# Performance work log

Hardware: AMD Instinct MI355X
Metric: run time of the kernel (lower is better)

## Reference

```python
import jax, jax.numpy as jnp
import numpy as np

N = 100_000      # nodes
E = 1_600_000    # edges (avg degree 16)
D_IN = 128
D_H = 128
D_P = 128
D_OUT = 64


def setup_inputs() -> dict:
    key = jax.random.key(0)
    ks = jax.random.split(key, 10)
    x = jax.random.normal(ks[0], (N, D_IN), dtype=jnp.float32)
    edge_index = jax.random.randint(ks[1], (2, E), 0, N, dtype=jnp.int64)
    # Mix_Pass layer 0: Linear(in->hidden, bias=False) + separate bias (zero-init)
    W1 = jax.random.normal(ks[2], (D_H, D_IN), dtype=jnp.float32) * 0.05
    b1 = jnp.zeros((D_H,), dtype=jnp.float32)
    # Mix_Pass layer 1: hidden->hidden
    W2 = jax.random.normal(ks[3], (D_H, D_H), dtype=jnp.float32) * 0.05
    b2 = jnp.zeros((D_H,), dtype=jnp.float32)
    # projection MLP
    fcW1 = jax.random.normal(ks[4], (D_P, D_H), dtype=jnp.float32) * 0.05
    fcb1 = jnp.zeros((D_P,), dtype=jnp.float32)
    fcW2 = jax.random.normal(ks[5], (D_OUT, D_P), dtype=jnp.float32) * 0.05
    fcb2 = jnp.zeros((D_OUT,), dtype=jnp.float32)
    return dict(x=x, edge_index=edge_index, W1=W1, b1=b1, W2=W2, b2=b2,
                fcW1=fcW1, fcb1=fcb1, fcW2=fcW2, fcb2=fcb2)


def _gcn_norm_with_self_loops(edge_index, n_nodes):
    # add_self_loops then gcn_norm (sym, improved=False, loops already added)
    loop = jnp.arange(n_nodes, dtype=edge_index.dtype)
    row = jnp.concatenate([edge_index[0], loop])  # source
    col = jnp.concatenate([edge_index[1], loop])  # target
    ew = jnp.ones(row.shape[0], dtype=jnp.float32)
    deg = jax.ops.segment_sum(ew, col, num_segments=n_nodes)
    dinv = jnp.where(deg > 0, jax.lax.rsqrt(deg), 0.0)
    return row, col, dinv[row] * ew * dinv[col]


def _mix_pass(z, W, b, row, col, ew, n_nodes):
    z = z @ W.T                                   # [N, out]
    msg = ew[:, None] * z[row]                    # gather source feats, scale
    out = jax.ops.segment_sum(msg, col, num_segments=n_nodes)  # scatter-add
    return out + b


def reference(x, edge_index, W1, b1, W2, b2, fcW1, fcb1, fcW2, fcb2):
    n_nodes = x.shape[0]
    row, col, ew = _gcn_norm_with_self_loops(edge_index, n_nodes)
    # dropout is identity in eval mode
    z = jax.nn.relu(_mix_pass(x, W1, b1, row, col, ew, n_nodes))
    zs = _mix_pass(z, W2, b2, row, col, ew, n_nodes)
    # project: elu(fc1) -> log_softmax(fc2)
    h = jax.nn.elu(zs @ fcW1.T + fcb1)
    res = jax.nn.log_softmax(h @ fcW2.T + fcb2, axis=1)
    return zs, res
```

## Files before the change

### kernel.cpp

```cpp
#include <hip/hip_runtime.h>
#include <hip/hip_bf16.h>

typedef __bf16 bf16_t;
typedef bf16_t bf16x8 __attribute__((ext_vector_type(8)));
typedef bf16_t bf16x4 __attribute__((ext_vector_type(4)));
typedef bf16_t bf16x2 __attribute__((ext_vector_type(2)));
typedef float f32x4 __attribute__((ext_vector_type(4)));

#define DEG_CAP 64

__device__ __forceinline__ void cvt4(const float* __restrict__ s, bf16_t* __restrict__ d, int i) {
    f32x4 v = ((const f32x4*)s)[i];
    bf16x4 o;
#pragma unroll
    for (int j = 0; j < 4; ++j) o[j] = (bf16_t)v[j];
    ((bf16x4*)d)[i] = o;
}

__global__ void setup_k(const float* xf, bf16_t* Xbf, int nx4,
                        const float* W1f, bf16_t* W1b,
                        const float* W2f, bf16_t* W2b,
                        const float* fW1f, bf16_t* fW1b,
                        const float* fW2f, bf16_t* fW2b,
                        int* cnt, int N) {
    int i = blockIdx.x * blockDim.x + threadIdx.x;
    if (i < nx4) { cvt4(xf, Xbf, i); return; }
    i -= nx4;
    if (i < 4096) { cvt4(W1f, W1b, i); return; }
    i -= 4096;
    if (i < 4096) { cvt4(W2f, W2b, i); return; }
    i -= 4096;
    if (i < 4096) { cvt4(fW1f, fW1b, i); return; }
    i -= 4096;
    if (i < 2048) { cvt4(fW2f, fW2b, i); return; }
    i -= 2048;
    if (i < N) cnt[i] = 0;
}

__device__ __forceinline__ void edge_rc(const int* __restrict__ ei, int E, int e,
                                        int N, int& r, int& c) {
    bool i64 = (ei[1] == 0) & (ei[3] == 0) & (ei[5] == 0) & (ei[7] == 0);
    int rr, cc;
    if (i64) { rr = ei[2 * e]; cc = ei[2 * E + 2 * e]; }
    else     { rr = ei[e];     cc = ei[E + e]; }
    r = ((unsigned)rr < (unsigned)N) ? rr : 0;
    c = ((unsigned)cc < (unsigned)N) ? cc : 0;
}

__global__ void countplace_k(const int* __restrict__ ei, int* __restrict__ cnt,
                             int* __restrict__ srcx, int E, int N) {
    int e = blockIdx.x * blockDim.x + threadIdx.x;
    if (e >= E) return;
    int r, c;
    edge_rc(ei, E, e, N, r, c);
    int p = atomicAdd(&cnt[c], 1);
    if (p < DEG_CAP) srcx[(size_t)c * DEG_CAP + p] = r;
}

template <int RELU, int WF32>
__global__ __launch_bounds__(256) void gather_k(const bf16_t* __restrict__ Y,
                                                const int* __restrict__ cnt,
                                                const int* __restrict__ srcx,
                                                const float* __restrict__ bias,
                                                bf16_t* __restrict__ out,
                                                float* __restrict__ out2, int n) {
    int node = blockIdx.x * 4 + (threadIdx.x >> 6);
    if (node >= n) return;
    int lane = threadIdx.x & 63;
    int f = lane * 2;
    int c = cnt[node];
    float di = rsqrtf((float)c + 1.0f);
    int cg = (c < DEG_CAP) ? c : DEG_CAP;
    const int* sl = srcx + (size_t)node * DEG_CAP;
    bf16x2 ys = *(const bf16x2*)(Y + (size_t)node * 128 + f);
    float a0 = (float)ys[0];
    float a1 = (float)ys[1];

    int e = 0;
    int end16 = cg & ~15;
    for (; e < end16; e += 16) {
        int s[16];
#pragma unroll
        for (int j = 0; j < 16; ++j) s[j] = sl[e + j];
        bf16x2 y[16];
#pragma unroll
        for (int j = 0; j < 16; ++j) y[j] = *(const bf16x2*)(Y + (size_t)s[j] * 128 + f);
#pragma unroll
        for (int j = 0; j < 16; ++j) { a0 += (float)y[j][0]; a1 += (float)y[j][1]; }
    }
    int end4 = cg & ~3;
    for (; e < end4; e += 4) {
        int s[4];
#pragma unroll
        for (int j = 0; j < 4; ++j) s[j] = sl[e + j];
        bf16x2 y[4];
#pragma unroll
        for (int j = 0; j < 4; ++j) y[j] = *(const bf16x2*)(Y + (size_t)s[j] * 128 + f);
#pragma unroll
        for (int j = 0; j < 4; ++j) { a0 += (float)y[j][0]; a1 += (float)y[j][1]; }
    }
    for (; e < cg; ++e) {
        bf16x2 y = *(const bf16x2*)(Y + (size_t)sl[e] * 128 + f);
        a0 += (float)y[0];
        a1 += (float)y[1];
    }

    a0 = di * a0 + bias[f];
    a1 = di * a1 + bias[f + 1];
    if (RELU) { a0 = fmaxf(a0, 0.0f); a1 = fmaxf(a1, 0.0f); }
    bf16x2 o;
    o[0] = (bf16_t)a0;
    o[1] = (bf16_t)a1;
    *(bf16x2*)(out + (size_t)node * 128 + f) = o;
    if (WF32) {
        out2[(size_t)node * 128 + f]     = a0;
        out2[(size_t)node * 128 + f + 1] = a1;
    }
}

template <int OC, int MODE, int MT>
__global__ __launch_bounds__(256) void gemm_k(const bf16_t* __restrict__ A,
                                              const bf16_t* __restrict__ W,
                                              const float* __restrict__ bias,
                                              const int* __restrict__ cnt,
                                              bf16_t* __restrict__ out,
                                              float* __restrict__ outf, int nrows) {
    const int lane = threadIdx.x & 63;
    const int wave = threadIdx.x >> 6;
    const int l16 = lane & 15;
    const int quad = lane >> 4;
    constexpr int NT = OC / 16;
    const int ntiles = (nrows + 15) >> 4;
    const int t0 = (blockIdx.x * 4 + wave) * MT;
    if (t0 >= ntiles) return;

    f32x4 acc[MT][NT];
#pragma unroll
    for (int mt = 0; mt < MT; ++mt)
#pragma unroll
        for (int n = 0; n < NT; ++n) acc[mt][n] = (f32x4){0.f, 0.f, 0.f, 0.f};

    const bf16_t* arow[MT];
#pragma unroll
    for (int mt = 0; mt < MT; ++mt) {
        int r = t0 * 16 + mt * 16 + l16;
        if (r > nrows - 1) r = nrows - 1;
        arow[mt] = A + (size_t)r * 128 + quad * 8;
    }
    const bf16_t* wrow = W + (size_t)l16 * 128 + quad * 8;

#pragma unroll
    for (int kt = 0; kt < 4; ++kt) {
        bf16x8 a[MT];
#pragma unroll
        for (int mt = 0; mt < MT; ++mt) a[mt] = *(const bf16x8*)(arow[mt] + kt * 32);
#pragma unroll
        for (int n = 0; n < NT; ++n) {
            bf16x8 b = *(const bf16x8*)(wrow + (size_t)n * 2048 + kt * 32);
#pragma unroll
            for (int mt = 0; mt < MT; ++mt)
                acc[mt][n] = __builtin_amdgcn_mfma_f32_16x16x32_bf16(a[mt], b, acc[mt][n], 0, 0, 0);
        }
    }

#pragma unroll
    for (int mt = 0; mt < MT; ++mt) {
        int m0 = (t0 + mt) * 16;
        if (m0 >= nrows) break;
        if constexpr (MODE == 0) {
#pragma unroll
            for (int r = 0; r < 4; ++r) {
                int row = m0 + quad * 4 + r;
                if (row < nrows) {
                    float sc = rsqrtf((float)cnt[row] + 1.0f);
#pragma unroll
                    for (int n = 0; n < NT; ++n)
                        out[(size_t)row * OC + n * 16 + l16] = (bf16_t)(sc * acc[mt][n][r]);
                }
            }
        } else if constexpr (MODE == 1) {
#pragma unroll
            for (int n = 0; n < NT; ++n) {
                float bb = bias[n * 16 + l16];
#pragma unroll
                for (int r = 0; r < 4; ++r) {
                    int row = m0 + quad * 4 + r;
                    float v = acc[mt][n][r] + bb;
                    v = (v > 0.0f) ? v : (expf(v) - 1.0f);
                    if (row < nrows)
                        out[(size_t)row * OC + n * 16 + l16] = (bf16_t)v;
                }
            }
        } else {
#pragma unroll
            for (int r = 0; r < 4; ++r) {
                float v[NT];
#pragma unroll
                for (int n = 0; n < NT; ++n) v[n] = acc[mt][n][r] + bias[n * 16 + l16];
                float mx = v[0];
#pragma unroll
                for (int n = 1; n < NT; ++n) mx = fmaxf(mx, v[n]);
#pragma unroll
                for (int m = 8; m >= 1; m >>= 1) mx = fmaxf(mx, __shfl_xor(mx, m));
                float s = 0.0f;
#pragma unroll
                for (int n = 0; n < NT; ++n) s += expf(v[n] - mx);
#pragma unroll
                for (int m = 8; m >= 1; m >>= 1) s += __shfl_xor(s, m);
                float lse = mx + logf(s);
                int row = m0 + quad * 4 + r;
                if (row < nrows)
#pragma unroll
                    for (int n = 0; n < NT; ++n)
                        outf[(size_t)row * OC + n * 16 + l16] = v[n] - lse;
            }
        }
    }
}

extern "C" void kernel_launch(void* const* d_in, const int* in_sizes, int n_in,
                              void* d_out, int out_size, void* d_ws, size_t ws_size,
                              hipStream_t stream) {
    const float* xf    = (const float*)d_in[0];
    const int*   ei    = (const int*)d_in[1];
    const float* W1f   = (const float*)d_in[2];
    const float* b1f   = (const float*)d_in[3];
    const float* W2f   = (const float*)d_in[4];
    const float* b2f   = (const float*)d_in[5];
    const float* fcW1f = (const float*)d_in[6];
    const float* fcb1f = (const float*)d_in[7];
    const float* fcW2f = (const float*)d_in[8];
    const float* fcb2f = (const float*)d_in[9];

    const int N = in_sizes[0] / 128;
    const int E = in_sizes[1] / 2;

    float* zs_out  = (float*)d_out;
    float* res_out = (float*)d_out + (size_t)N * 128;

    char* ws = (char*)d_ws;
    size_t o = 0;
    auto carve = [&](size_t bytes) { void* p = ws + o; o = (o + bytes + 255) & ~255UL; return p; };
    int*    cnt    = (int*)carve((size_t)N * 4);
    int*    srcx   = (int*)carve((size_t)N * DEG_CAP * 4);
    bf16_t* Xbf    = (bf16_t*)carve((size_t)N * 128 * 2);
    bf16_t* Ybf    = (bf16_t*)carve((size_t)N * 128 * 2);
    bf16_t* W1b    = (bf16_t*)carve(128 * 128 * 2);
    bf16_t* W2b    = (bf16_t*)carve(128 * 128 * 2);
    bf16_t* fW1b   = (bf16_t*)carve(128 * 128 * 2);
    bf16_t* fW2b   = (bf16_t*)carve(64 * 128 * 2);

    const int B = 256;
    const int ntiles = (N + 15) / 16;
    const int gblocks = (ntiles + 15) / 16;
    const int nodeblocks = (N + 3) / 4;
    const int nx4 = N * 32;
    const int nsetup = nx4 + 4096 * 3 + 2048 + N;

    setup_k<<<(nsetup + B - 1) / B, B, 0, stream>>>(xf, Xbf, nx4, W1f, W1b, W2f, W2b,
                                                    fcW1f, fW1b, fcW2f, fW2b, cnt, N);
    countplace_k<<<(E + B - 1) / B, B, 0, stream>>>(ei, cnt, srcx, E, N);

    gemm_k<128, 0, 4><<<gblocks, B, 0, stream>>>(Xbf, W1b, nullptr, cnt, Ybf, nullptr, N);
    gather_k<1, 0><<<nodeblocks, B, 0, stream>>>(Ybf, cnt, srcx, b1f, Xbf, nullptr, N);

    gemm_k<128, 0, 4><<<gblocks, B, 0, stream>>>(Xbf, W2b, nullptr, cnt, Ybf, nullptr, N);
    gather_k<0, 1><<<nodeblocks, B, 0, stream>>>(Ybf, cnt, srcx, b2f, Xbf, zs_out, N);

    gemm_k<128, 1, 4><<<gblocks, B, 0, stream>>>(Xbf, fW1b, fcb1f, nullptr, Ybf, nullptr, N);
    gemm_k<64, 2, 4><<<gblocks, B, 0, stream>>>(Ybf, fW2b, fcb2f, nullptr, nullptr, res_out, N);
}
```

Measured before the change: 482.5 us.

## Gather 16-byte rows with four edges per wave and zero-row padding

```diff
diff --git a/kernel.cpp b/kernel.cpp
--- a/kernel.cpp
+++ b/kernel.cpp
@@ -22,7 +22,7 @@
                         const float* W2f, bf16_t* W2b,
                         const float* fW1f, bf16_t* fW1b,
                         const float* fW2f, bf16_t* fW2b,
-                        int* cnt, int N) {
+                        int* cnt, int N, int* yzero) {
     int i = blockIdx.x * blockDim.x + threadIdx.x;
     if (i < nx4) { cvt4(xf, Xbf, i); return; }
     i -= nx4;
@@ -34,7 +34,9 @@
     i -= 4096;
     if (i < 2048) { cvt4(fW2f, fW2b, i); return; }
     i -= 2048;
-    if (i < N) cnt[i] = 0;
+    if (i < N) { cnt[i] = 0; return; }
+    i -= N;
+    if (i < 64) yzero[i] = 0;
 }
 
 __device__ __forceinline__ void edge_rc(const int* __restrict__ ei, int E, int e,
@@ -67,54 +69,66 @@
     int node = blockIdx.x * 4 + (threadIdx.x >> 6);
     if (node >= n) return;
     int lane = threadIdx.x & 63;
-    int f = lane * 2;
+    int l16 = lane & 15;
+    int quad = lane >> 4;
     int c = cnt[node];
     float di = rsqrtf((float)c + 1.0f);
     int cg = (c < DEG_CAP) ? c : DEG_CAP;
     const int* sl = srcx + (size_t)node * DEG_CAP;
-    bf16x2 ys = *(const bf16x2*)(Y + (size_t)node * 128 + f);
-    float a0 = (float)ys[0];
-    float a1 = (float)ys[1];
-
-    int e = 0;
-    int end16 = cg & ~15;
-    for (; e < end16; e += 16) {
-        int s[16];
-#pragma unroll
-        for (int j = 0; j < 16; ++j) s[j] = sl[e + j];
-        bf16x2 y[16];
-#pragma unroll
-        for (int j = 0; j < 16; ++j) y[j] = *(const bf16x2*)(Y + (size_t)s[j] * 128 + f);
-#pragma unroll
-        for (int j = 0; j < 16; ++j) { a0 += (float)y[j][0]; a1 += (float)y[j][1]; }
-    }
-    int end4 = cg & ~3;
-    for (; e < end4; e += 4) {
-        int s[4];
-#pragma unroll
-        for (int j = 0; j < 4; ++j) s[j] = sl[e + j];
-        bf16x2 y[4];
-#pragma unroll
-        for (int j = 0; j < 4; ++j) y[j] = *(const bf16x2*)(Y + (size_t)s[j] * 128 + f);
-#pragma unroll
-        for (int j = 0; j < 4; ++j) { a0 += (float)y[j][0]; a1 += (float)y[j][1]; }
-    }
-    for (; e < cg; ++e) {
-        bf16x2 y = *(const bf16x2*)(Y + (size_t)sl[e] * 128 + f);
-        a0 += (float)y[0];
-        a1 += (float)y[1];
-    }
-
-    a0 = di * a0 + bias[f];
-    a1 = di * a1 + bias[f + 1];
-    if (RELU) { a0 = fmaxf(a0, 0.0f); a1 = fmaxf(a1, 0.0f); }
-    bf16x2 o;
-    o[0] = (bf16_t)a0;
-    o[1] = (bf16_t)a1;
-    *(bf16x2*)(out + (size_t)node * 128 + f) = o;
+    const bf16_t* Yl = Y + l16 * 8;
+
+    bf16x8 ys = *(const bf16x8*)(Yl + (size_t)node * 128);
+
+    float acc[8];
+#pragma unroll
+    for (int j = 0; j < 8; ++j) acc[j] = 0.f;
+
+    for (int e = 0; e < cg; e += 16) {
+        int4 sq = *(const int4*)(sl + e + quad * 4);
+        int idx0 = e + quad * 4;
+        int s0 = (idx0 + 0 < cg) ? sq.x : n;
+        int s1 = (idx0 + 1 < cg) ? sq.y : n;
+        int s2 = (idx0 + 2 < cg) ? sq.z : n;
+        int s3 = (idx0 + 3 < cg) ? sq.w : n;
+        bf16x8 y0 = *(const bf16x8*)(Yl + (size_t)s0 * 128);
+        bf16x8 y1 = *(const bf16x8*)(Yl + (size_t)s1 * 128);
+        bf16x8 y2 = *(const bf16x8*)(Yl + (size_t)s2 * 128);
+        bf16x8 y3 = *(const bf16x8*)(Yl + (size_t)s3 * 128);
+#pragma unroll
+        for (int j = 0; j < 8; ++j)
+            acc[j] += (float)y0[j] + (float)y1[j] + (float)y2[j] + (float)y3[j];
+    }
+
+#pragma unroll
+    for (int j = 0; j < 8; ++j) {
+        acc[j] += __shfl_xor(acc[j], 16);
+        acc[j] += __shfl_xor(acc[j], 32);
+    }
+
+    f32x4 b0 = ((const f32x4*)bias)[l16 * 2];
+    f32x4 b1 = ((const f32x4*)bias)[l16 * 2 + 1];
+    float v[8];
+#pragma unroll
+    for (int j = 0; j < 8; ++j) {
+        float bb = (j < 4) ? b0[j & 3] : b1[j & 3];
+        v[j] = di * ((float)ys[j] + acc[j]) + bb;
+        if (RELU) v[j] = fmaxf(v[j], 0.f);
+    }
+
+    if (quad == 0) {
+        bf16x8 o;
+#pragma unroll
+        for (int j = 0; j < 8; ++j) o[j] = (bf16_t)v[j];
+        *(bf16x8*)(out + (size_t)node * 128 + l16 * 8) = o;
+    }
     if (WF32) {
-        out2[(size_t)node * 128 + f]     = a0;
-        out2[(size_t)node * 128 + f + 1] = a1;
+        if (quad == 1) {
+            f32x4 w = {v[0], v[1], v[2], v[3]};
+            *(f32x4*)(out2 + (size_t)node * 128 + l16 * 8) = w;
+        } else if (quad == 2) {
+            f32x4 w = {v[4], v[5], v[6], v[7]};
+            *(f32x4*)(out2 + (size_t)node * 128 + l16 * 8 + 4) = w;
+        }
     }
 }
 
@@ -244,7 +258,7 @@
     int*    cnt    = (int*)carve((size_t)N * 4);
     int*    srcx   = (int*)carve((size_t)N * DEG_CAP * 4);
     bf16_t* Xbf    = (bf16_t*)carve((size_t)N * 128 * 2);
-    bf16_t* Ybf    = (bf16_t*)carve((size_t)N * 128 * 2);
+    bf16_t* Ybf    = (bf16_t*)carve((size_t)(N + 1) * 128 * 2);
     bf16_t* W1b    = (bf16_t*)carve(128 * 128 * 2);
     bf16_t* W2b    = (bf16_t*)carve(128 * 128 * 2);
     bf16_t* fW1b   = (bf16_t*)carve(128 * 128 * 2);
@@ -255,10 +269,11 @@
     const int gblocks = (ntiles + 15) / 16;
     const int nodeblocks = (N + 3) / 4;
     const int nx4 = N * 32;
-    const int nsetup = nx4 + 4096 * 3 + 2048 + N;
+    const int nsetup = nx4 + 4096 * 3 + 2048 + N + 64;
 
     setup_k<<<(nsetup + B - 1) / B, B, 0, stream>>>(xf, Xbf, nx4, W1f, W1b, W2f, W2b,
-                                                    fcW1f, fW1b, fcW2f, fW2b, cnt, N);
+                                                    fcW1f, fW1b, fcW2f, fW2b, cnt, N,
+                                                    (int*)(Ybf + (size_t)N * 128));
     countplace_k<<<(E + B - 1) / B, B, 0, stream>>>(ei, cnt, srcx, E, N);
 
     gemm_k<128, 0, 4><<<gblocks, B, 0, stream>>>(Xbf, W1b, nullptr, cnt, Ybf, nullptr, N);
```

After: 477.7 us. About the same (-1.0%).
